# Kernel optimization log

Measured on AMD Instinct MI355X. Metric: run time of the kernel, lower is better.

The kernel has to match this reference:

```python
import jax, jax.numpy as jnp
import numpy as np

IMAGE_SIZE = 256


def setup_inputs():
    B, A, S, C = 2, 3, 8, 20
    key = jax.random.key(0)
    k1, k2, k3, k4, k5, k6 = jax.random.split(key, 6)
    predictions = jax.random.normal(k1, (B, A, S, S, 6 + C), dtype=jnp.float32)
    obj = (jax.random.uniform(k2, (B, A, S, S)) < 0.15).astype(jnp.float32)
    txy = jax.random.uniform(k3, (B, A, S, S, 2), minval=0.05, maxval=0.95)
    twh = jax.random.uniform(k4, (B, A, S, S, 2), minval=0.3, maxval=3.0)
    cls = jax.random.randint(k5, (B, A, S, S), 0, C).astype(jnp.float32)
    target = jnp.concatenate([obj[..., None], txy, twh, cls[..., None]], axis=-1)
    anchors = jnp.array([[0.9, 1.6], [2.2, 3.0], [4.8, 6.1]], dtype=jnp.float32)
    depth_target = jax.random.uniform(k6, (B, IMAGE_SIZE, IMAGE_SIZE), minval=0.0, maxval=80.0)
    return {"predictions": predictions, "target": target, "anchors": anchors,
            "depth_target": depth_target, "S": S}


def _bce_logits_masked(x, y, m):
    # BCEWithLogitsLoss (mean) restricted to mask m
    l = jnp.maximum(x, 0.0) - x * y + jnp.log1p(jnp.exp(-jnp.abs(x)))
    mf = m.astype(x.dtype)
    return (l * mf).sum() / jnp.maximum(mf.sum(), 1.0)


def _iou_midpoint(a, b):
    ax1, ax2 = a[..., 0] - a[..., 2] / 2, a[..., 0] + a[..., 2] / 2
    ay1, ay2 = a[..., 1] - a[..., 3] / 2, a[..., 1] + a[..., 3] / 2
    bx1, bx2 = b[..., 0] - b[..., 2] / 2, b[..., 0] + b[..., 2] / 2
    by1, by2 = b[..., 1] - b[..., 3] / 2, b[..., 1] + b[..., 3] / 2
    iw = jnp.clip(jnp.minimum(ax2, bx2) - jnp.maximum(ax1, bx1), 0.0)
    ih = jnp.clip(jnp.minimum(ay2, by2) - jnp.maximum(ay1, by1), 0.0)
    inter = iw * ih
    area_a = jnp.abs((ax2 - ax1) * (ay2 - ay1))
    area_b = jnp.abs((bx2 - bx1) * (by2 - by1))
    return inter / (area_a + area_b - inter + 1e-6)


def _silog_masked(pred, tgt, m):
    # SILogLoss with boolean mask; torch.var is unbiased (n-1)
    mf = m.astype(jnp.float32)
    n = mf.sum()
    g = (jnp.log(jnp.maximum(pred, 1e-30)) - jnp.log(jnp.maximum(tgt, 1e-30))) * mf
    mean = g.sum() / jnp.maximum(n, 1.0)
    var = (((g - mean) ** 2) * mf).sum() / jnp.maximum(n - 1.0, 1.0)
    Dg = var + 0.15 * mean ** 2
    return 10.0 * jnp.sqrt(jnp.maximum(Dg, 1e-30)), n


def _axis_mask(lo, hi, L):
    # replicate python slice semantics a[int(lo):int(hi)] (trunc toward 0, negative wrap)
    lo = jnp.trunc(jnp.clip(lo, -1e9, 1e9)).astype(jnp.int32)
    hi = jnp.trunc(jnp.clip(hi, -1e9, 1e9)).astype(jnp.int32)
    lo = jnp.where(lo < 0, jnp.maximum(L + lo, 0), jnp.minimum(lo, L))
    hi = jnp.where(hi < 0, jnp.maximum(L + hi, 0), jnp.minimum(hi, L))
    r = jnp.arange(L)
    return (r >= lo) & (r < hi)


def reference(predictions, target, anchors, depth_target, S):
    B, A = predictions.shape[0], predictions.shape[1]
    IMG = depth_target.shape[-1]
    objf = (target[..., 0] == 1.0).astype(jnp.float32)
    noobj = target[..., 0] == 0.0
    n_obj = jnp.maximum(objf.sum(), 1.0)

    no_object_loss = _bce_logits_masked(predictions[..., 0], target[..., 0], noobj)

    anch = anchors.reshape(1, A, 1, 1, 2)
    box_preds = jnp.concatenate([jax.nn.sigmoid(predictions[..., 1:3]),
                                 jnp.exp(predictions[..., 3:5]) * anch], axis=-1)
    ious = jax.lax.stop_gradient(_iou_midpoint(box_preds, target[..., 1:5]))
    object_loss = (((jax.nn.sigmoid(predictions[..., 0]) - ious * target[..., 0]) ** 2) * objf).sum() / n_obj

    # in-place mutation in original: predictions[...,1:3] = sigmoid(...)
    pred_xy = jax.nn.sigmoid(predictions[..., 1:3])
    tgt_box = jnp.concatenate([target[..., 1:3], jnp.log(1e-16 + target[..., 3:5] / anch)], axis=-1)
    pred_box = jnp.concatenate([pred_xy, predictions[..., 3:5]], axis=-1)
    box_loss = (((pred_box - tgt_box) ** 2) * objf[..., None]).sum() / (n_obj * 4.0)

    logp = jax.nn.log_softmax(predictions[..., 6:], axis=-1)
    labels = target[..., 5].astype(jnp.int32)
    nll = -jnp.take_along_axis(logp, labels[..., None], axis=-1)[..., 0]
    class_loss = (nll * objf).sum() / n_obj

    # depth rasterization loop; cells_to_bboxes mutates predictions in place, so
    # each outer k iteration compounds sigmoid on xy and exp*anchor on wh
    xy, wh = pred_xy, predictions[..., 3:5]
    cxs, cys, ws, hs, vs = [], [], [], [], []
    jj = jnp.arange(S)[None, None, None, :].astype(jnp.float32)
    ii = jnp.arange(S)[None, None, :, None].astype(jnp.float32)
    for k in range(A):
        xy = jax.nn.sigmoid(xy)
        wh = jnp.exp(wh) * anch
        cx = (xy[..., 0] + jj) / S * IMG
        cy = (xy[..., 1] + ii) / S * IMG
        w = wh[..., 0] / S * IMG
        h = wh[..., 1] / S * IMG
        # loop order in source: k, i, j, b -> layout [S, S, B] per k
        cxs.append(jnp.transpose(cx[:, k], (1, 2, 0)))
        cys.append(jnp.transpose(cy[:, k], (1, 2, 0)))
        ws.append(jnp.transpose(w[:, k], (1, 2, 0)))
        hs.append(jnp.transpose(h[:, k], (1, 2, 0)))
        vs.append(jnp.transpose(predictions[:, k, :, :, 5], (1, 2, 0)))
    floats = jnp.stack([jnp.stack(cxs).ravel(), jnp.stack(cys).ravel(),
                        jnp.stack(ws).ravel(), jnp.stack(hs).ravel(),
                        jnp.stack(vs).ravel()], axis=-1)  # [T,5]
    bidx = jnp.broadcast_to(jnp.arange(B), (A, S, S, B)).reshape(-1)

    @jax.checkpoint
    def step(carry, inp):
        dp, ds, loss, cnt = carry
        f, b = inp
        cx, cy, w, h, v = f[0], f[1], f[2], f[3], f[4]
        valid = (w > 0) & (h > 0) & jnp.isfinite(w) & jnp.isfinite(h)
        val = jnp.maximum(1.0, v)
        bm = (jnp.arange(B) == b)[:, None, None]
        rf = _axis_mask(cx - w / 2, cx + w / 2, IMG)[:, None] & _axis_mask(cy - h / 2, cy + h / 2, IMG)[None, :]
        rs = _axis_mask(cx - w / 4, cx + w / 4, IMG)[:, None] & _axis_mask(cy - h / 4, cy + h / 4, IMG)[None, :]
        dp = jnp.where(valid & bm & rf[None], val, dp)
        ds = jnp.where(valid & bm & rs[None], val, ds)
        mf = (depth_target >= 1.0) & (dp >= 1.0)
        pl1, n1 = _silog_masked(dp, depth_target, mf)
        add1 = valid & (n1 >= 2.0)  # n==1 -> unbiased var NaN -> skipped in torch
        loss = loss + jnp.where(add1, pl1, 0.0)
        cnt = cnt + add1.astype(jnp.float32)
        ms = (depth_target >= 1.0) & (ds >= 1.0)
        pl2, n2 = _silog_masked(ds, depth_target, ms)
        add2 = valid & (n2 >= 2.0)
        loss = loss + jnp.where(add2, pl2, 0.0)
        cnt = cnt + add2.astype(jnp.float32)
        return (dp, ds, loss, cnt), None

    init = (jnp.zeros_like(depth_target), jnp.zeros_like(depth_target),
            jnp.float32(0.0), jnp.float32(0.0))
    (_, _, dloss, cnt), _ = jax.lax.scan(step, init, (floats, bidx))
    depth_loss = dloss / jnp.maximum(cnt, 1.0)

    return (10.0 * box_loss + 1.0 * object_loss + 10.0 * no_object_loss
            + 1.0 * class_loss + 1.0 * depth_loss)
```

## Files before the change

### kernel.cpp

```cpp
#include <hip/hip_runtime.h>
#include <cmath>

#define BN 2
#define AN 3
#define SN 8
#define CN 20
#define IMGN 256
#define NSTEP 384
#define PRED_C 26
#define NE (NSTEP * 6)
#define NB (BN * IMGN)
#define NSB (NSTEP / BN)

__device__ __forceinline__ float wredf(float v){
  #pragma unroll
  for (int o = 32; o; o >>= 1) v += __shfl_xor(v, o);
  return v;
}
__device__ __forceinline__ double wredd(double v){
  #pragma unroll
  for (int o = 32; o; o >>= 1) v += __shfl_xor(v, o);
  return v;
}
__device__ __forceinline__ float wsum_dpp(float x){
  x += __int_as_float(__builtin_amdgcn_update_dpp(0, __float_as_int(x), 0x111, 0xf, 0xf, false));
  x += __int_as_float(__builtin_amdgcn_update_dpp(0, __float_as_int(x), 0x112, 0xf, 0xf, false));
  x += __int_as_float(__builtin_amdgcn_update_dpp(0, __float_as_int(x), 0x114, 0xf, 0xf, false));
  x += __int_as_float(__builtin_amdgcn_update_dpp(0, __float_as_int(x), 0x118, 0xf, 0xf, false));
  x += __int_as_float(__builtin_amdgcn_update_dpp(0, __float_as_int(x), 0x142, 0xa, 0xf, false));
  x += __int_as_float(__builtin_amdgcn_update_dpp(0, __float_as_int(x), 0x143, 0xc, 0xf, false));
  return x;
}
__device__ __forceinline__ int finitef(float x){
  return (__float_as_uint(x) & 0x7f800000u) != 0x7f800000u;
}
__device__ __forceinline__ unsigned axism(float lo, float hi){
  float lof = truncf(fminf(fmaxf(lo, -1e9f), 1e9f));
  float hif = truncf(fminf(fmaxf(hi, -1e9f), 1e9f));
  int l = (int)lof, h = (int)hif;
  l = (l < 0) ? max(IMGN + l, 0) : min(l, IMGN);
  h = (h < 0) ? max(IMGN + h, 0) : min(h, IMGN);
  return (unsigned)l | ((unsigned)h << 16);
}

__device__ __forceinline__ void step_params(int t, const float* __restrict__ pred,
                                            const float* __restrict__ anc,
                                            unsigned* valid, float* lv,
                                            unsigned* fx, unsigned* fy,
                                            unsigned* sx, unsigned* sy){
  int b = t % BN;
  int j = (t / BN) % SN;
  int i = (t / (BN * SN)) % SN;
  int k = t / (BN * SN * SN);
  const float* pc = pred + (size_t)((((b * AN + k) * SN + i) * SN + j)) * PRED_C;
  float x = pc[1], y = pc[2], wv = pc[3], hv = pc[4], v = pc[5];
  float aw = anc[2 * k], ah = anc[2 * k + 1];
  for (int m = 0; m < k + 2; ++m) {
    x = 1.0f / (1.0f + expf(-x));
    y = 1.0f / (1.0f + expf(-y));
  }
  for (int m = 0; m < k + 1; ++m) {
    wv = expf(wv) * aw;
    hv = expf(hv) * ah;
  }
  float cx = (x + (float)j) / 8.0f * 256.0f;
  float cy = (y + (float)i) / 8.0f * 256.0f;
  float w  = wv / 8.0f * 256.0f;
  float h  = hv / 8.0f * 256.0f;
  *valid = (w > 0.0f) && (h > 0.0f) && finitef(w) && finitef(h);
  *lv = logf(fmaxf(1.0f, v));
  *fx = axism(cx - w / 2.0f, cx + w / 2.0f);
  *fy = axism(cy - h / 2.0f, cy + h / 2.0f);
  *sx = axism(cx - w / 4.0f, cx + w / 4.0f);
  *sy = axism(cy - h / 4.0f, cy + h / 4.0f);
}

__global__ __launch_bounds__(256) void yolo_kB(const float* __restrict__ pred,
                                               const float* __restrict__ anc,
                                               const float* __restrict__ depth,
                                               float* __restrict__ scratch){
  __shared__ uint2    s_rxx[NSTEP];
  __shared__ uint2    s_cyy[NSTEP];
  __shared__ float    s_lv[NSTEP];
  __shared__ unsigned s_list[4][NSB];
  __shared__ int      s_nact[4];
  __shared__ float    s_acc[NE];

  int tid = threadIdx.x;
  for (int t = tid; t < NSTEP; t += 256) {
    unsigned vld, fx, fy, sx, sy; float lv;
    step_params(t, pred, anc, &vld, &lv, &fx, &fy, &sx, &sy);
    if (!vld) { fx = 0xFFFFu; sx = 0xFFFFu; }
    s_rxx[t] = make_uint2(fx, sx);
    s_cyy[t] = make_uint2(fy, sy);
    s_lv[t] = lv;
  }
  for (int e = tid; e < NE; e += 256) s_acc[e] = 0.0f;
  __syncthreads();

  int ru = blockIdx.x;
  int b = ru >> 8, r = ru & 255;
  int c = tid, ln = tid & 63, w = tid >> 6;
  int wlo = w * 64, whi = wlo + 64;

  {
    int cnt = 0;
    #pragma unroll
    for (int g = 0; g < 3; ++g) {
      int m = g * 64 + ln;
      int t = b + 2 * m;
      uint2 rx = s_rxx[t];
      uint2 cy = s_cyy[t];
      bool rowF = (r >= (int)(rx.x & 0xffffu)) && (r < (int)(rx.x >> 16));
      bool rowS = (r >= (int)(rx.y & 0xffffu)) && (r < (int)(rx.y >> 16));
      bool fF = rowF && ((int)(cy.x & 0xffffu) < whi) && ((int)(cy.x >> 16) > wlo);
      bool fS = rowS && ((int)(cy.y & 0xffffu) < whi) && ((int)(cy.y >> 16) > wlo);
      bool f = fF || fS;
      unsigned long long msk = __ballot(f);
      int pos = (int)__popcll(msk & ((1ull << ln) - 1ull));
      if (f) s_list[w][cnt + pos] = (unsigned)t | (fF ? 512u : 0u) | (fS ? 1024u : 0u);
      cnt += (int)__popcll(msk);
    }
    if (ln == 0) s_nact[w] = cnt;
  }

  float dt = depth[(size_t)ru * IMGN + c];
  bool okp = dt >= 1.0f;
  float ldt = okp ? logf(dt) : 0.0f;
  __syncthreads();
  int nact = s_nact[w];

  bool hF = false, hS = false;
  float lvF = ldt, lvS = ldt;
  float ldt2 = 2.0f * ldt;
  #pragma unroll 2
  for (int idx = 0; idx < nact; ++idx) {
    unsigned ent = s_list[w][idx];
    int t = (int)(ent & 511u);
    uint2 cyb = s_cyy[t];
    float lv = s_lv[t];
    bool inF = (ent & 512u)  && okp && (c >= (int)(cyb.x & 0xffffu)) && (c < (int)(cyb.x >> 16));
    bool inS = (ent & 1024u) && okp && (c >= (int)(cyb.y & 0xffffu)) && (c < (int)(cyb.y >> 16));
    unsigned long long mF = __ballot(inF && !hF);
    unsigned long long mS = __ballot(inS && !hS);
    hF |= inF; hS |= inS;
    float d1 = inF ? (lv - lvF) : 0.0f;
    float d2 = d1 * (lv + lvF - ldt2);
    lvF = inF ? lv : lvF;
    float e1 = inS ? (lv - lvS) : 0.0f;
    float e2 = e1 * (lv + lvS - ldt2);
    lvS = inS ? lv : lvS;
    d1 = wsum_dpp(d1); d2 = wsum_dpp(d2);
    e1 = wsum_dpp(e1); e2 = wsum_dpp(e2);
    if (ln == 63) {
      float* base = s_acc + t * 6;
      float c0 = (float)__popcll(mF), c3 = (float)__popcll(mS);
      if (c0 != 0.f) atomicAdd(base + 0, c0);
      if (d1 != 0.f) atomicAdd(base + 1, d1);
      if (d2 != 0.f) atomicAdd(base + 2, d2);
      if (c3 != 0.f) atomicAdd(base + 3, c3);
      if (e1 != 0.f) atomicAdd(base + 4, e1);
      if (e2 != 0.f) atomicAdd(base + 5, e2);
    }
  }
  __syncthreads();
  for (int e = tid; e < NE; e += 256)
    scratch[(size_t)blockIdx.x * NE + e] = s_acc[e];
}

__global__ __launch_bounds__(256) void yolo_kR(const float* __restrict__ scratch,
                                               double* __restrict__ reduced){
  __shared__ double part[4][64];
  int ln = threadIdx.x & 63, w = threadIdx.x >> 6;
  int e = blockIdx.x * 64 + ln;
  double s = 0.0;
  for (int bk = w * (NB / 4); bk < (w + 1) * (NB / 4); ++bk)
    s += (double)scratch[(size_t)bk * NE + e];
  part[w][ln] = s;
  __syncthreads();
  if (w == 0)
    reduced[e] = part[0][ln] + part[1][ln] + part[2][ln] + part[3][ln];
}

__global__ __launch_bounds__(384) void yolo_kC(const float* __restrict__ pred,
                                               const float* __restrict__ tgt,
                                               const float* __restrict__ anc,
                                               const double* __restrict__ reduced,
                                               float* __restrict__ out){
  __shared__ double sd[NE];
  __shared__ double chunk[6 * 6];
  __shared__ double rl[6], rc[6];
  __shared__ float  ry[6 * 6];
  int tid = threadIdx.x;
  for (int e = tid; e < NE; e += 384) sd[e] = reduced[e];

  float s_obj, s_bce, s_bcecnt, s_objls, s_boxls, s_clsls;
  {
    int t = tid;
    int j = t % SN;
    int i = (t / SN) % SN;
    int a = (t / (SN * SN)) % AN;
    int b = t / (SN * SN * AN);
    const float* pc = pred + (size_t)((((b * AN + a) * SN + i) * SN + j)) * PRED_C;
    const float* tc = tgt  + (size_t)((((b * AN + a) * SN + i) * SN + j)) * 6;
    float t0 = tc[0];
    float objf  = (t0 == 1.0f) ? 1.0f : 0.0f;
    float noobj = (t0 == 0.0f) ? 1.0f : 0.0f;
    float p0 = pc[0];
    float l = fmaxf(p0, 0.0f) - p0 * t0 + log1pf(expf(-fabsf(p0)));
    s_bce = l * noobj; s_bcecnt = noobj; s_obj = objf;
    float aw = anc[2 * a], ah = anc[2 * a + 1];
    float sxp = 1.0f / (1.0f + expf(-pc[1]));
    float syp = 1.0f / (1.0f + expf(-pc[2]));
    float bw = expf(pc[3]) * aw, bh = expf(pc[4]) * ah;
    float ax1 = sxp - bw * 0.5f, ax2 = sxp + bw * 0.5f;
    float ay1 = syp - bh * 0.5f, ay2 = syp + bh * 0.5f;
    float bx1 = tc[1] - tc[3] * 0.5f, bx2 = tc[1] + tc[3] * 0.5f;
    float by1 = tc[2] - tc[4] * 0.5f, by2 = tc[2] + tc[4] * 0.5f;
    float iw = fmaxf(fminf(ax2, bx2) - fmaxf(ax1, bx1), 0.0f);
    float ih = fmaxf(fminf(ay2, by2) - fmaxf(ay1, by1), 0.0f);
    float inter = iw * ih;
    float areaA = fabsf((ax2 - ax1) * (ay2 - ay1));
    float areaB = fabsf((bx2 - bx1) * (by2 - by1));
    float iou = inter / (areaA + areaB - inter + 1e-6f);
    float sp0 = 1.0f / (1.0f + expf(-p0));
    float od = sp0 - iou * t0;
    s_objls = od * od * objf;
    float dx = sxp - tc[1], dy = syp - tc[2];
    float dw = pc[3] - logf(1e-16f + tc[3] / aw);
    float dh = pc[4] - logf(1e-16f + tc[4] / ah);
    s_boxls = (dx * dx + dy * dy + dw * dw + dh * dh) * objf;
    int lbl = (int)tc[5];
    float mx = -INFINITY;
    for (int c = 0; c < CN; ++c) mx = fmaxf(mx, pc[6 + c]);
    float se = 0.0f;
    for (int c = 0; c < CN; ++c) se += expf(pc[6 + c] - mx);
    float nll = mx + logf(se) - pc[6 + lbl];
    s_clsls = nll * objf;
  }
  {
    int wv = tid >> 6, ln = tid & 63;
    float vals[6] = { s_obj, s_bce, s_bcecnt, s_objls, s_boxls, s_clsls };
    #pragma unroll
    for (int ci = 0; ci < 6; ++ci) {
      float v = wredf(vals[ci]);
      if (ln == 0) ry[ci * 6 + wv] = v;
    }
  }

  unsigned vld, ufx, ufy, usx, usy; float ulv;
  step_params(tid, pred, anc, &vld, &ulv, &ufx, &ufy, &usx, &usy);

  __syncthreads();
  {
    int ch = tid >> 6, ln = tid & 63;
    #pragma unroll
    for (int comp = 0; comp < 6; ++comp) {
      double v = wredd(sd[(ch * 64 + ln) * 6 + comp]);
      if (ln == 0) chunk[ch * 6 + comp] = v;
    }
  }
  __syncthreads();

  int t = tid;
  int ch = t >> 6;
  double P[6];
  #pragma unroll
  for (int comp = 0; comp < 6; ++comp) {
    double s = 0.0;
    for (int cc = 0; cc < ch; ++cc) s += chunk[cc * 6 + comp];
    for (int tt = (ch << 6); tt <= t; ++tt) s += sd[tt * 6 + comp];
    P[comp] = s;
  }
  double lossd = 0.0, cntd = 0.0;
  {
    double n = P[0], Sg = P[1], Sg2 = P[2];
    double mean = Sg / fmax(n, 1.0);
    double var = (Sg2 - 2.0 * mean * Sg + n * mean * mean) / fmax(n - 1.0, 1.0);
    double Dg = var + 0.15 * mean * mean;
    double pl = 10.0 * sqrt(fmax(Dg, 1e-30));
    if (vld && n >= 2.0) { lossd += pl; cntd += 1.0; }
  }
  {
    double n = P[3], Sg = P[4], Sg2 = P[5];
    double mean = Sg / fmax(n, 1.0);
    double var = (Sg2 - 2.0 * mean * Sg + n * mean * mean) / fmax(n - 1.0, 1.0);
    double Dg = var + 0.15 * mean * mean;
    double pl = 10.0 * sqrt(fmax(Dg, 1e-30));
    if (vld && n >= 2.0) { lossd += pl; cntd += 1.0; }
  }
  int wv = tid >> 6, ln = tid & 63;
  double L = wredd(lossd), C = wredd(cntd);
  if (ln == 0) { rl[wv] = L; rc[wv] = C; }
  __syncthreads();
  if (tid == 0) {
    double totL = 0.0, totC = 0.0;
    for (int i = 0; i < 6; ++i) { totL += rl[i]; totC += rc[i]; }
    float yolo[6];
    #pragma unroll
    for (int ci = 0; ci < 6; ++ci) {
      float s = 0.0f;
      for (int w2 = 0; w2 < 6; ++w2) s += ry[ci * 6 + w2];
      yolo[ci] = s;
    }
    float dl = (float)(totL / fmax(totC, 1.0));
    float nobj = fmaxf(yolo[0], 1.0f);
    float noo  = yolo[1] / fmaxf(yolo[2], 1.0f);
    float objl = yolo[3] / nobj;
    float boxl = yolo[4] / (nobj * 4.0f);
    float clsl = yolo[5] / nobj;
    out[0] = 10.0f * boxl + objl + 10.0f * noo + clsl + dl;
  }
}

extern "C" void kernel_launch(void* const* d_in, const int* in_sizes, int n_in,
                              void* d_out, int out_size, void* d_ws, size_t ws_size,
                              hipStream_t stream) {
  const float* pred  = (const float*)d_in[0];
  const float* tgt   = (const float*)d_in[1];
  const float* anc   = (const float*)d_in[2];
  const float* depth = (const float*)d_in[3];

  float* scratch = (float*)d_ws;
  double* reduced = (double*)((char*)d_ws + (size_t)NB * NE * sizeof(float));

  hipLaunchKernelGGL(yolo_kB, dim3(NB), dim3(256), 0, stream, pred, anc, depth, scratch);
  hipLaunchKernelGGL(yolo_kR, dim3(NE / 64), dim3(256), 0, stream, scratch, reduced);
  hipLaunchKernelGGL(yolo_kC, dim3(1), dim3(384), 0, stream, pred, tgt, anc, reduced, (float*)d_out);
}
```

Before: 122.2 us.

## Process two image rows per block and fuse reduction with final loss kernel

Result: slower. 129.4 us (+5.9%).

```diff
diff --git a/kernel.cpp b/kernel.cpp
--- a/kernel.cpp
+++ b/kernel.cpp
@@ -9,8 +9,9 @@
 #define NSTEP 384
 #define PRED_C 26
 #define NE (NSTEP * 6)
-#define NB (BN * IMGN)
+#define NBB 256
 #define NSB (NSTEP / BN)
+#define NRB 36
 
 __device__ __forceinline__ float wredf(float v){
   #pragma unroll
@@ -75,19 +76,22 @@
   *sy = axism(cy - h / 4.0f, cy + h / 4.0f);
 }
 
-__global__ __launch_bounds__(256) void yolo_kB(const float* __restrict__ pred,
+__global__ __launch_bounds__(512) void yolo_kB(const float* __restrict__ pred,
                                                const float* __restrict__ anc,
                                                const float* __restrict__ depth,
-                                               float* __restrict__ scratch){
+                                               float* __restrict__ scratch,
+                                               unsigned* __restrict__ ctr){
   __shared__ uint2    s_rxx[NSTEP];
   __shared__ uint2    s_cyy[NSTEP];
   __shared__ float    s_lv[NSTEP];
-  __shared__ unsigned s_list[4][NSB];
-  __shared__ int      s_nact[4];
+  __shared__ unsigned s_list[8][NSB];
+  __shared__ int      s_nact[8];
   __shared__ float    s_acc[NE];
 
   int tid = threadIdx.x;
-  for (int t = tid; t < NSTEP; t += 256) {
+  if (blockIdx.x == 0 && tid == 0) *ctr = 0u;
+
+  for (int t = tid; t < NSTEP; t += 512) {
     unsigned vld, fx, fy, sx, sy; float lv;
     step_params(t, pred, anc, &vld, &lv, &fx, &fy, &sx, &sy);
     if (!vld) { fx = 0xFFFFu; sx = 0xFFFFu; }
@@ -95,13 +99,14 @@
     s_cyy[t] = make_uint2(fy, sy);
     s_lv[t] = lv;
   }
-  for (int e = tid; e < NE; e += 256) s_acc[e] = 0.0f;
-  __syncthreads();
-
-  int ru = blockIdx.x;
+  for (int e = tid; e < NE; e += 512) s_acc[e] = 0.0f;
+  __syncthreads();
+
+  int half = tid >> 8;
+  int ru = blockIdx.x * 2 + half;
   int b = ru >> 8, r = ru & 255;
-  int c = tid, ln = tid & 63, w = tid >> 6;
-  int wlo = w * 64, whi = wlo + 64;
+  int c = tid & 255, ln = tid & 63, w = tid >> 6;
+  int wlo = c & ~63, whi = wlo + 64;
 
   {
     int cnt = 0;
@@ -164,35 +169,54 @@
     }
   }
   __syncthreads();
-  for (int e = tid; e < NE; e += 256)
+  for (int e = tid; e < NE; e += 512)
     scratch[(size_t)blockIdx.x * NE + e] = s_acc[e];
 }
 
-__global__ __launch_bounds__(256) void yolo_kR(const float* __restrict__ scratch,
-                                               double* __restrict__ reduced){
-  __shared__ double part[4][64];
-  int ln = threadIdx.x & 63, w = threadIdx.x >> 6;
-  int e = blockIdx.x * 64 + ln;
-  double s = 0.0;
-  for (int bk = w * (NB / 4); bk < (w + 1) * (NB / 4); ++bk)
-    s += (double)scratch[(size_t)bk * NE + e];
-  part[w][ln] = s;
-  __syncthreads();
-  if (w == 0)
-    reduced[e] = part[0][ln] + part[1][ln] + part[2][ln] + part[3][ln];
-}
-
-__global__ __launch_bounds__(384) void yolo_kC(const float* __restrict__ pred,
-                                               const float* __restrict__ tgt,
-                                               const float* __restrict__ anc,
-                                               const double* __restrict__ reduced,
-                                               float* __restrict__ out){
+__global__ __launch_bounds__(384) void yolo_kRC(const float* __restrict__ pred,
+                                                const float* __restrict__ tgt,
+                                                const float* __restrict__ anc,
+                                                const float* __restrict__ scratch,
+                                                double* __restrict__ reduced,
+                                                unsigned* __restrict__ ctr,
+                                                float* __restrict__ out){
+  __shared__ double part[6][64];
+  __shared__ int s_last;
+  int tid = threadIdx.x;
+  int ln = tid & 63, grp = tid >> 6;
+
+  {
+    int e = blockIdx.x * 64 + ln;
+    const int CH = (NBB + 5) / 6;
+    int bk0 = grp * CH, bk1 = min(NBB, bk0 + CH);
+    double s = 0.0;
+    for (int bk = bk0; bk < bk1; ++bk)
+      s += (double)scratch[(size_t)bk * NE + e];
+    part[grp][ln] = s;
+  }
+  __syncthreads();
+  if (grp == 0) {
+    int e = blockIdx.x * 64 + ln;
+    double s = part[0][ln] + part[1][ln] + part[2][ln] +
+               part[3][ln] + part[4][ln] + part[5][ln];
+    __hip_atomic_store(&reduced[e], s, __ATOMIC_RELEASE, __HIP_MEMORY_SCOPE_AGENT);
+  }
+  __syncthreads();
+  if (tid == 0) {
+    __threadfence();
+    unsigned old = __hip_atomic_fetch_add(ctr, 1u, __ATOMIC_ACQ_REL, __HIP_MEMORY_SCOPE_AGENT);
+    s_last = (old == NRB - 1);
+  }
+  __syncthreads();
+  if (!s_last) return;
+  __threadfence();
+
   __shared__ double sd[NE];
   __shared__ double chunk[6 * 6];
   __shared__ double rl[6], rc[6];
   __shared__ float  ry[6 * 6];
-  int tid = threadIdx.x;
-  for (int e = tid; e < NE; e += 384) sd[e] = reduced[e];
+  for (int e = tid; e < NE; e += 384)
+    sd[e] = __hip_atomic_load(&reduced[e], __ATOMIC_ACQUIRE, __HIP_MEMORY_SCOPE_AGENT);
 
   float s_obj, s_bce, s_bcecnt, s_objls, s_boxls, s_clsls;
   {
@@ -239,12 +263,11 @@
     s_clsls = nll * objf;
   }
   {
-    int wv = tid >> 6, ln = tid & 63;
     float vals[6] = { s_obj, s_bce, s_bcecnt, s_objls, s_boxls, s_clsls };
     #pragma unroll
     for (int ci = 0; ci < 6; ++ci) {
       float v = wredf(vals[ci]);
-      if (ln == 0) ry[ci * 6 + wv] = v;
+      if (ln == 0) ry[ci * 6 + grp] = v;
     }
   }
 
@@ -253,11 +276,10 @@
 
   __syncthreads();
   {
-    int ch = tid >> 6, ln = tid & 63;
     #pragma unroll
     for (int comp = 0; comp < 6; ++comp) {
-      double v = wredd(sd[(ch * 64 + ln) * 6 + comp]);
-      if (ln == 0) chunk[ch * 6 + comp] = v;
+      double v = wredd(sd[(grp * 64 + ln) * 6 + comp]);
+      if (ln == 0) chunk[grp * 6 + comp] = v;
     }
   }
   __syncthreads();
@@ -289,9 +311,8 @@
     double pl = 10.0 * sqrt(fmax(Dg, 1e-30));
     if (vld && n >= 2.0) { lossd += pl; cntd += 1.0; }
   }
-  int wv = tid >> 6, ln = tid & 63;
   double L = wredd(lossd), C = wredd(cntd);
-  if (ln == 0) { rl[wv] = L; rc[wv] = C; }
+  if (ln == 0) { rl[grp] = L; rc[grp] = C; }
   __syncthreads();
   if (tid == 0) {
     double totL = 0.0, totC = 0.0;
@@ -321,10 +342,11 @@
   const float* anc   = (const float*)d_in[2];
   const float* depth = (const float*)d_in[3];
 
-  float* scratch = (float*)d_ws;
-  double* reduced = (double*)((char*)d_ws + (size_t)NB * NE * sizeof(float));
-
-  hipLaunchKernelGGL(yolo_kB, dim3(NB), dim3(256), 0, stream, pred, anc, depth, scratch);
-  hipLaunchKernelGGL(yolo_kR, dim3(NE / 64), dim3(256), 0, stream, scratch, reduced);
-  hipLaunchKernelGGL(yolo_kC, dim3(1), dim3(384), 0, stream, pred, tgt, anc, reduced, (float*)d_out);
-}
+  float*    scratch = (float*)d_ws;
+  double*   reduced = (double*)((char*)d_ws + (size_t)NBB * NE * sizeof(float));
+  unsigned* ctr     = (unsigned*)((char*)reduced + (size_t)NE * sizeof(double));
+
+  hipLaunchKernelGGL(yolo_kB, dim3(NBB), dim3(512), 0, stream, pred, anc, depth, scratch, ctr);
+  hipLaunchKernelGGL(yolo_kRC, dim3(NRB), dim3(384), 0, stream, pred, tgt, anc,
+                     scratch, reduced, ctr, (float*)d_out);
+}
```

## Process two rows per block and pack candidate list entries with bounds

Applied to the files above, without the earlier changes.

Result: slower. 133.2 us (+9.0%).

```diff
diff --git a/kernel.cpp b/kernel.cpp
--- a/kernel.cpp
+++ b/kernel.cpp
@@ -9,8 +9,9 @@
 #define NSTEP 384
 #define PRED_C 26
 #define NE (NSTEP * 6)
-#define NB (BN * IMGN)
+#define NBB 256
 #define NSB (NSTEP / BN)
+#define NRB 36
 
 __device__ __forceinline__ float wredf(float v){
   #pragma unroll
@@ -75,19 +76,19 @@
   *sy = axism(cy - h / 4.0f, cy + h / 4.0f);
 }
 
-__global__ __launch_bounds__(256) void yolo_kB(const float* __restrict__ pred,
+__global__ __launch_bounds__(512) void yolo_kB(const float* __restrict__ pred,
                                                const float* __restrict__ anc,
                                                const float* __restrict__ depth,
                                                float* __restrict__ scratch){
   __shared__ uint2    s_rxx[NSTEP];
   __shared__ uint2    s_cyy[NSTEP];
   __shared__ float    s_lv[NSTEP];
-  __shared__ unsigned s_list[4][NSB];
-  __shared__ int      s_nact[4];
+  __shared__ uint4    s_clist[8][NSB];
+  __shared__ int      s_nact[8];
   __shared__ float    s_acc[NE];
 
   int tid = threadIdx.x;
-  for (int t = tid; t < NSTEP; t += 256) {
+  for (int t = tid; t < NSTEP; t += 512) {
     unsigned vld, fx, fy, sx, sy; float lv;
     step_params(t, pred, anc, &vld, &lv, &fx, &fy, &sx, &sy);
     if (!vld) { fx = 0xFFFFu; sx = 0xFFFFu; }
@@ -95,13 +96,14 @@
     s_cyy[t] = make_uint2(fy, sy);
     s_lv[t] = lv;
   }
-  for (int e = tid; e < NE; e += 256) s_acc[e] = 0.0f;
-  __syncthreads();
-
-  int ru = blockIdx.x;
+  for (int e = tid; e < NE; e += 512) s_acc[e] = 0.0f;
+  __syncthreads();
+
+  int half = tid >> 8;
+  int ru = blockIdx.x * 2 + half;
   int b = ru >> 8, r = ru & 255;
-  int c = tid, ln = tid & 63, w = tid >> 6;
-  int wlo = w * 64, whi = wlo + 64;
+  int c = tid & 255, ln = tid & 63, w = tid >> 6;
+  int wlo = c & ~63, whi = wlo + 64;
 
   {
     int cnt = 0;
@@ -118,7 +120,10 @@
       bool f = fF || fS;
       unsigned long long msk = __ballot(f);
       int pos = (int)__popcll(msk & ((1ull << ln) - 1ull));
-      if (f) s_list[w][cnt + pos] = (unsigned)t | (fF ? 512u : 0u) | (fS ? 1024u : 0u);
+      if (f) {
+        unsigned tf = (unsigned)t | (fF ? 512u : 0u) | (fS ? 1024u : 0u);
+        s_clist[w][cnt + pos] = make_uint4(cy.x, cy.y, __float_as_uint(s_lv[t]), tf);
+      }
       cnt += (int)__popcll(msk);
     }
     if (ln == 0) s_nact[w] = cnt;
@@ -127,44 +132,47 @@
   float dt = depth[(size_t)ru * IMGN + c];
   bool okp = dt >= 1.0f;
   float ldt = okp ? logf(dt) : 0.0f;
+  int ce = okp ? c : 0x7fffffff;
   __syncthreads();
   int nact = s_nact[w];
 
   bool hF = false, hS = false;
   float lvF = ldt, lvS = ldt;
   float ldt2 = 2.0f * ldt;
-  #pragma unroll 2
+  uint4 cur = (nact > 0) ? s_clist[w][0] : make_uint4(0u, 0u, 0u, 0u);
   for (int idx = 0; idx < nact; ++idx) {
-    unsigned ent = s_list[w][idx];
-    int t = (int)(ent & 511u);
-    uint2 cyb = s_cyy[t];
-    float lv = s_lv[t];
-    bool inF = (ent & 512u)  && okp && (c >= (int)(cyb.x & 0xffffu)) && (c < (int)(cyb.x >> 16));
-    bool inS = (ent & 1024u) && okp && (c >= (int)(cyb.y & 0xffffu)) && (c < (int)(cyb.y >> 16));
-    unsigned long long mF = __ballot(inF && !hF);
-    unsigned long long mS = __ballot(inS && !hS);
-    hF |= inF; hS |= inS;
-    float d1 = inF ? (lv - lvF) : 0.0f;
-    float d2 = d1 * (lv + lvF - ldt2);
-    lvF = inF ? lv : lvF;
-    float e1 = inS ? (lv - lvS) : 0.0f;
-    float e2 = e1 * (lv + lvS - ldt2);
-    lvS = inS ? lv : lvS;
-    d1 = wsum_dpp(d1); d2 = wsum_dpp(d2);
-    e1 = wsum_dpp(e1); e2 = wsum_dpp(e2);
-    if (ln == 63) {
-      float* base = s_acc + t * 6;
-      float c0 = (float)__popcll(mF), c3 = (float)__popcll(mS);
-      if (c0 != 0.f) atomicAdd(base + 0, c0);
-      if (d1 != 0.f) atomicAdd(base + 1, d1);
-      if (d2 != 0.f) atomicAdd(base + 2, d2);
-      if (c3 != 0.f) atomicAdd(base + 3, c3);
-      if (e1 != 0.f) atomicAdd(base + 4, e1);
-      if (e2 != 0.f) atomicAdd(base + 5, e2);
-    }
-  }
-  __syncthreads();
-  for (int e = tid; e < NE; e += 256)
+    uint4 nxt = (idx + 1 < nact) ? s_clist[w][idx + 1] : cur;
+    unsigned tf = cur.w;
+    float lv = __uint_as_float(cur.z);
+    bool inF = (tf & 512u)  && (ce >= (int)(cur.x & 0xffffu)) && (ce < (int)(cur.x >> 16));
+    bool inS = (tf & 1024u) && (ce >= (int)(cur.y & 0xffffu)) && (ce < (int)(cur.y >> 16));
+    if (__ballot(inF || inS) != 0ull) {
+      unsigned long long mF = __ballot(inF && !hF);
+      unsigned long long mS = __ballot(inS && !hS);
+      hF |= inF; hS |= inS;
+      float d1 = inF ? (lv - lvF) : 0.0f;
+      float d2 = d1 * (lv + lvF - ldt2);
+      lvF = inF ? lv : lvF;
+      float g1 = inS ? (lv - lvS) : 0.0f;
+      float g2 = g1 * (lv + lvS - ldt2);
+      lvS = inS ? lv : lvS;
+      d1 = wsum_dpp(d1); d2 = wsum_dpp(d2);
+      g1 = wsum_dpp(g1); g2 = wsum_dpp(g2);
+      if (ln == 63) {
+        float* base = s_acc + (int)(tf & 511u) * 6;
+        float c0 = (float)__popcll(mF), c3 = (float)__popcll(mS);
+        if (c0 != 0.f) atomicAdd(base + 0, c0);
+        if (d1 != 0.f) atomicAdd(base + 1, d1);
+        if (d2 != 0.f) atomicAdd(base + 2, d2);
+        if (c3 != 0.f) atomicAdd(base + 3, c3);
+        if (g1 != 0.f) atomicAdd(base + 4, g1);
+        if (g2 != 0.f) atomicAdd(base + 5, g2);
+      }
+    }
+    cur = nxt;
+  }
+  __syncthreads();
+  for (int e = tid; e < NE; e += 512)
     scratch[(size_t)blockIdx.x * NE + e] = s_acc[e];
 }
 
@@ -174,7 +182,7 @@
   int ln = threadIdx.x & 63, w = threadIdx.x >> 6;
   int e = blockIdx.x * 64 + ln;
   double s = 0.0;
-  for (int bk = w * (NB / 4); bk < (w + 1) * (NB / 4); ++bk)
+  for (int bk = w * (NBB / 4); bk < (w + 1) * (NBB / 4); ++bk)
     s += (double)scratch[(size_t)bk * NE + e];
   part[w][ln] = s;
   __syncthreads();
@@ -321,10 +329,10 @@
   const float* anc   = (const float*)d_in[2];
   const float* depth = (const float*)d_in[3];
 
-  float* scratch = (float*)d_ws;
-  double* reduced = (double*)((char*)d_ws + (size_t)NB * NE * sizeof(float));
-
-  hipLaunchKernelGGL(yolo_kB, dim3(NB), dim3(256), 0, stream, pred, anc, depth, scratch);
-  hipLaunchKernelGGL(yolo_kR, dim3(NE / 64), dim3(256), 0, stream, scratch, reduced);
+  float*  scratch = (float*)d_ws;
+  double* reduced = (double*)((char*)d_ws + (size_t)NBB * NE * sizeof(float));
+
+  hipLaunchKernelGGL(yolo_kB, dim3(NBB), dim3(512), 0, stream, pred, anc, depth, scratch);
+  hipLaunchKernelGGL(yolo_kR, dim3(NRB), dim3(256), 0, stream, scratch, reduced);
   hipLaunchKernelGGL(yolo_kC, dim3(1), dim3(384), 0, stream, pred, tgt, anc, reduced, (float*)d_out);
 }
```
